# Optimization experiments

Hardware: AMD Instinct MI355X
Metric: run time of the kernel (lower is better)

## Reference

```python
import jax, jax.numpy as jnp
import numpy as np

T, B, H, I = 128, 128, 256, 256


def setup_inputs() -> dict:
    key = jax.random.key(0)
    ks = jax.random.split(key, 8)
    s = 1.0 / np.sqrt(H)
    embs = jax.random.normal(ks[0], (T, B, I), jnp.float32)
    # lens in [1, T] (a length of 0 is meaningless for this module)
    lens = jnp.maximum(jax.random.randint(ks[1], (B,), 0, T + 1), 1)
    Wih = jax.random.uniform(ks[2], (4 * H, I), jnp.float32, -s, s)
    Whh = jax.random.uniform(ks[3], (4 * H, H), jnp.float32, -s, s)
    bih = jax.random.uniform(ks[4], (4 * H,), jnp.float32, -s, s)
    bhh = jax.random.uniform(ks[5], (4 * H,), jnp.float32, -s, s)
    Wa = jax.random.uniform(ks[6], (H, 2 * H), jnp.float32, -s, s)
    ba = jnp.zeros((H,), jnp.float32)
    return {"embs": embs, "lens": lens, "Wih": Wih, "Whh": Whh,
            "bih": bih, "bhh": bhh, "Wa": Wa, "ba": ba}


def _forward(embs, Wih, Whh, bih, bhh, Wa, ba):
    Tn, Bn, _ = embs.shape
    Hn = Whh.shape[1]
    h0 = jnp.zeros((Bn, Hn), embs.dtype)
    c0 = jnp.zeros((Bn, Hn), embs.dtype)
    hids0 = jnp.zeros((Tn, Bn, Hn), embs.dtype)  # growing history of outputs
    pos = jnp.arange(Tn)

    def step(carry, emb):
        h, c, hids, t = carry
        # attention of current hidden over all previous outputs (dot-product scores)
        scores = jnp.einsum('bh,tbh->tb', h, hids)          # [T,B]
        valid = pos[:, None] < jnp.maximum(t, 1)             # at least one valid slot avoids NaN
        scores = jnp.where(valid, scores, -1e30)
        w = jax.nn.softmax(scores, axis=0)
        ctx = jnp.einsum('tb,tbh->bh', w, hids)              # [B,H]
        h_att = jnp.tanh(jnp.concatenate([h, ctx], axis=-1) @ Wa.T + ba)
        h_in = jnp.where(t > 0, h_att, h)                    # no attention before first output
        # one LSTM cell step (PyTorch gate order: i, f, g, o)
        gates = emb @ Wih.T + bih + h_in @ Whh.T + bhh       # [B,4H]
        i, f, g, o = jnp.split(gates, 4, axis=-1)
        c_new = jax.nn.sigmoid(f) * c + jax.nn.sigmoid(i) * jnp.tanh(g)
        h_new = jax.nn.sigmoid(o) * jnp.tanh(c_new)
        hids = jax.lax.dynamic_update_slice(hids, h_new[None], (t, 0, 0))
        return (h_new, c_new, hids, t + 1), (h_new, c_new)

    _, (hs, cs) = jax.lax.scan(step, (h0, c0, hids0, jnp.int32(0)), embs)
    return hs, cs  # each [T,B,H]


def reference(embs, lens, Wih, Whh, bih, bhh, Wa, ba):
    hs, cs = _forward(embs, Wih, Whh, bih, bhh, Wa, ba)
    bidx = jnp.arange(hs.shape[1])
    h_fin = hs[lens - 1, bidx][None]  # [1,B,H], state at t == len-1
    c_fin = cs[lens - 1, bidx][None]
    return hs, h_fin, c_fin
```

## Files before the change

### kernel.cpp

```cpp
#include <hip/hip_runtime.h>
#include <math.h>

#define T 128
#define B 128
#define H 256
#define I 256
#define G4 1024

typedef unsigned short u16;
typedef unsigned int u32;

__device__ __forceinline__ float2 bf2_to_f2(u32 u) {
    union { u32 i; float f; } a, b;
    a.i = u << 16;
    b.i = u & 0xffff0000u;
    return make_float2(a.f, b.f);
}

__device__ __forceinline__ u16 bf16_rne(float f) {
    union { float f; u32 u; } x; x.f = f;
    u32 r = x.u + 0x7fffu + ((x.u >> 16) & 1u);
    return (u16)(r >> 16);
}

__device__ __forceinline__ float sigmoid_fast(float x) {
    return 1.0f / (1.0f + __expf(-x));
}
__device__ __forceinline__ float tanh_fast(float x) {
    x = fminf(fmaxf(x, -15.f), 15.f);
    const float e = __expf(2.0f * x);
    return (e - 1.0f) / (e + 1.0f);
}

__global__ void pack_whB(const float* __restrict__ Whh, u16* __restrict__ WhB) {
    const int k = blockIdx.x;
    const int o = threadIdx.x;
    WhB[(size_t)k * G4 + o] = bf16_rne(Whh[(size_t)o * H + k]);
}
__global__ void pack_waB(const float* __restrict__ Wa, u16* __restrict__ WaB) {
    const int k = blockIdx.x;
    const int j = threadIdx.x;
    WaB[(size_t)k * H + j] = bf16_rne(Wa[(size_t)j * (2 * H) + k]);
}

__global__ __launch_bounds__(256) void gemm_g(const float* __restrict__ A,
                                              const float* __restrict__ W,
                                              const float* __restrict__ bih,
                                              const float* __restrict__ bhh,
                                              float* __restrict__ G) {
    __shared__ __align__(16) float As[64][68];
    __shared__ __align__(16) float Ws[64][68];
    const int m0 = blockIdx.x * 64;
    const int n0 = blockIdx.y * 64;
    const int tid = threadIdx.x;
    const int ty = tid >> 4, tx = tid & 15;
    const int rr = tid >> 4;
    const int kr = tid & 15;

    float acc[4][4] = {};
    for (int k0 = 0; k0 < I; k0 += 64) {
#pragma unroll
        for (int i = 0; i < 4; ++i) {
            const int r = rr + 16 * i;
            const float4 av = *(const float4*)&A[(size_t)(m0 + r) * I + k0 + kr * 4];
            const float4 wv = *(const float4*)&W[(size_t)(n0 + r) * I + k0 + kr * 4];
            As[kr * 4 + 0][r] = av.x; As[kr * 4 + 1][r] = av.y;
            As[kr * 4 + 2][r] = av.z; As[kr * 4 + 3][r] = av.w;
            Ws[kr * 4 + 0][r] = wv.x; Ws[kr * 4 + 1][r] = wv.y;
            Ws[kr * 4 + 2][r] = wv.z; Ws[kr * 4 + 3][r] = wv.w;
        }
        __syncthreads();
#pragma unroll 8
        for (int kk = 0; kk < 64; ++kk) {
            const float4 a4 = *(const float4*)&As[kk][ty * 4];
            const float4 w4 = *(const float4*)&Ws[kk][tx * 4];
            const float a[4] = {a4.x, a4.y, a4.z, a4.w};
            const float w[4] = {w4.x, w4.y, w4.z, w4.w};
#pragma unroll
            for (int i = 0; i < 4; ++i)
#pragma unroll
                for (int jj = 0; jj < 4; ++jj)
                    acc[i][jj] = fmaf(a[i], w[jj], acc[i][jj]);
        }
        __syncthreads();
    }
    const int n = n0 + tx * 4;
    const float4 bi = *(const float4*)&bih[n];
    const float4 bh = *(const float4*)&bhh[n];
    const float4 bb = make_float4(bi.x + bh.x, bi.y + bh.y, bi.z + bh.z, bi.w + bh.w);
#pragma unroll
    for (int i = 0; i < 4; ++i) {
        const int m = m0 + ty * 4 + i;
        float4 o = make_float4(acc[i][0] + bb.x, acc[i][1] + bb.y,
                               acc[i][2] + bb.z, acc[i][3] + bb.w);
        *(float4*)&G[(size_t)m * G4 + n] = o;
    }
}

__global__ __launch_bounds__(1024, 4) void alstm2(
    const int* __restrict__ lens,
    const float* __restrict__ G,
    const u16* __restrict__ WhB,
    const u16* __restrict__ WaB,
    const float* __restrict__ ba,
    float* __restrict__ out)
{
    __shared__ __align__(16) float hid_s[T][H];
    __shared__ __align__(16) float red_s[4096];
    __shared__ __align__(16) float gate_s[G4];
    __shared__ __align__(16) float h_s[H];
    __shared__ __align__(16) float hin_s[H];
    __shared__ __align__(16) float ctx_s[H];
    __shared__ __align__(16) float sc_s[T];

    const int b = blockIdx.x;
    const int tid = threadIdx.x;
    const int lane = tid & 63;
    const int wave = tid >> 6;
    const int len_b = lens[b];

    const int ko_h = tid >> 8;
    const int jo_h = tid & 255;
    const int ko_a = tid >> 6;
    const int jo_a = tid & 63;

    float c_reg = 0.f;
    const float ba_j = (tid < H) ? ba[tid] : 0.f;
    if (tid < H) h_s[tid] = 0.f;
    float* hs_out = out;
    float* hfin = out + (size_t)T * B * H;
    float* cfin = hfin + (size_t)B * H;
    __syncthreads();

    for (int t = 0; t < T; ++t) {
        if (t > 0) {
            const float4 h4 = *(const float4*)&h_s[lane * 4];
            for (int tp = wave; tp < t; tp += 16) {
                const float4 hv = *(const float4*)&hid_s[tp][lane * 4];
                float d = hv.x * h4.x + hv.y * h4.y + hv.z * h4.z + hv.w * h4.w;
#pragma unroll
                for (int off = 32; off; off >>= 1) d += __shfl_xor(d, off);
                if (lane == 0) sc_s[tp] = d;
            }
            __syncthreads();
            if (wave == 0) {
                const float v0 = (lane < t) ? sc_s[lane] : -3.0e38f;
                const float v1 = (lane + 64 < t) ? sc_s[lane + 64] : -3.0e38f;
                float m = fmaxf(v0, v1);
#pragma unroll
                for (int off = 32; off; off >>= 1) m = fmaxf(m, __shfl_xor(m, off));
                const float e0 = (lane < t) ? __expf(v0 - m) : 0.f;
                const float e1 = (lane + 64 < t) ? __expf(v1 - m) : 0.f;
                float s = e0 + e1;
#pragma unroll
                for (int off = 32; off; off >>= 1) s += __shfl_xor(s, off);
                const float inv = 1.f / s;
                if (lane < t) sc_s[lane] = e0 * inv;
                if (lane + 64 < t) sc_s[lane + 64] = e1 * inv;
            }
            __syncthreads();
            {
                float cacc = 0.f;
                for (int tp = ko_h; tp < t; tp += 4)
                    cacc = fmaf(sc_s[tp], hid_s[tp][jo_h], cacc);
                red_s[ko_h * H + jo_h] = cacc;
            }
            __syncthreads();
            if (tid < H)
                ctx_s[tid] = red_s[tid] + red_s[H + tid] + red_s[2 * H + tid] + red_s[3 * H + tid];
            __syncthreads();
            {
                float a0 = 0.f, a1 = 0.f, a2 = 0.f, a3 = 0.f;
                const int kb = ko_a * 32;
#pragma unroll 8
                for (int kk = 0; kk < 32; ++kk) {
                    const int k = kb + kk;
                    const float vin = (k < H) ? h_s[k] : ctx_s[k - H];
                    const uint2 w = *(const uint2*)&WaB[(size_t)k * H + jo_a * 4];
                    const float2 w01 = bf2_to_f2(w.x), w23 = bf2_to_f2(w.y);
                    a0 = fmaf(w01.x, vin, a0); a1 = fmaf(w01.y, vin, a1);
                    a2 = fmaf(w23.x, vin, a2); a3 = fmaf(w23.y, vin, a3);
                }
                *(float4*)&red_s[ko_a * H + jo_a * 4] = make_float4(a0, a1, a2, a3);
            }
            __syncthreads();
            if (tid < H) {
                float a = ba_j;
#pragma unroll
                for (int r = 0; r < 16; ++r) a += red_s[r * H + tid];
                hin_s[tid] = tanh_fast(a);
            }
        } else {
            if (tid < H) hin_s[tid] = 0.f;
        }
        __syncthreads();
        {
            float g0 = 0.f, g1 = 0.f, g2 = 0.f, g3 = 0.f;
            const int kb = ko_h * 64;
#pragma unroll 8
            for (int kk = 0; kk < 64; ++kk) {
                const int k = kb + kk;
                const float hk = hin_s[k];
                const uint2 w = *(const uint2*)&WhB[(size_t)k * G4 + jo_h * 4];
                const float2 w01 = bf2_to_f2(w.x), w23 = bf2_to_f2(w.y);
                g0 = fmaf(w01.x, hk, g0); g1 = fmaf(w01.y, hk, g1);
                g2 = fmaf(w23.x, hk, g2); g3 = fmaf(w23.y, hk, g3);
            }
            *(float4*)&red_s[ko_h * G4 + jo_h * 4] = make_float4(g0, g1, g2, g3);
        }
        __syncthreads();
        {
            const float* Grow = G + (size_t)(t * B + b) * G4;
            gate_s[tid] = Grow[tid] + red_s[tid] + red_s[G4 + tid]
                        + red_s[2 * G4 + tid] + red_s[3 * G4 + tid];
        }
        __syncthreads();
        if (tid < H) {
            const float ig = sigmoid_fast(gate_s[tid]);
            const float fg = sigmoid_fast(gate_s[H + tid]);
            const float gg = tanh_fast(gate_s[2 * H + tid]);
            const float og = sigmoid_fast(gate_s[3 * H + tid]);
            c_reg = fmaf(fg, c_reg, ig * gg);
            const float h_new = og * tanh_fast(c_reg);
            h_s[tid] = h_new;
            hid_s[t][tid] = h_new;
            hs_out[(size_t)(t * B + b) * H + tid] = h_new;
            if (t == len_b - 1) {
                hfin[b * H + tid] = h_new;
                cfin[b * H + tid] = c_reg;
            }
        }
        __syncthreads();
    }
}

extern "C" void kernel_launch(void* const* d_in, const int* in_sizes, int n_in,
                              void* d_out, int out_size, void* d_ws, size_t ws_size,
                              hipStream_t stream) {
    const float* embs = (const float*)d_in[0];
    const int*   lens = (const int*)d_in[1];
    const float* Wih  = (const float*)d_in[2];
    const float* Whh  = (const float*)d_in[3];
    const float* bih  = (const float*)d_in[4];
    const float* bhh  = (const float*)d_in[5];
    const float* Wa   = (const float*)d_in[6];
    const float* ba   = (const float*)d_in[7];
    float* out = (float*)d_out;

    float* G  = (float*)d_ws;
    u16* WhB  = (u16*)(G + (size_t)T * B * G4);
    u16* WaB  = WhB + (size_t)H * G4;

    pack_whB<<<H, G4, 0, stream>>>(Whh, WhB);
    pack_waB<<<2 * H, H, 0, stream>>>(Wa, WaB);
    dim3 ggrid(T * B / 64, G4 / 64);
    gemm_g<<<ggrid, 256, 0, stream>>>(embs, Wih, bih, bhh, G);
    alstm2<<<B, 1024, 0, stream>>>(lens, G, WhB, WaB, ba, out);
}
```

Measured before the change: 2.078 ms.

## Process two batch rows per block with bf16 history and shared weight loads

```diff
diff --git a/kernel.cpp b/kernel.cpp
--- a/kernel.cpp
+++ b/kernel.cpp
@@ -6,6 +6,7 @@
 #define H 256
 #define I 256
 #define G4 1024
+#define NB 2
 
 typedef unsigned short u16;
 typedef unsigned int u32;
@@ -16,13 +17,14 @@
     b.i = u & 0xffff0000u;
     return make_float2(a.f, b.f);
 }
-
+__device__ __forceinline__ float bf1_to_f(u16 u) {
+    union { u32 i; float f; } a; a.i = ((u32)u) << 16; return a.f;
+}
 __device__ __forceinline__ u16 bf16_rne(float f) {
     union { float f; u32 u; } x; x.f = f;
     u32 r = x.u + 0x7fffu + ((x.u >> 16) & 1u);
     return (u16)(r >> 16);
 }
-
 __device__ __forceinline__ float sigmoid_fast(float x) {
     return 1.0f / (1.0f + __expf(-x));
 }
@@ -97,7 +99,7 @@
     }
 }
 
-__global__ __launch_bounds__(1024, 4) void alstm2(
+__global__ __launch_bounds__(1024, 4) void alstm3(
     const int* __restrict__ lens,
     const float* __restrict__ G,
     const u16* __restrict__ WhB,
@@ -105,47 +107,56 @@
     const float* __restrict__ ba,
     float* __restrict__ out)
 {
-    __shared__ __align__(16) float hid_s[T][H];
+    __shared__ __align__(16) u16   hid_s[NB][T][H];
     __shared__ __align__(16) float red_s[4096];
-    __shared__ __align__(16) float gate_s[G4];
-    __shared__ __align__(16) float h_s[H];
-    __shared__ __align__(16) float hin_s[H];
-    __shared__ __align__(16) float ctx_s[H];
-    __shared__ __align__(16) float sc_s[T];
-
-    const int b = blockIdx.x;
+    __shared__ __align__(16) float gate_s[NB][G4];
+    __shared__ __align__(16) float h_s[NB][H];
+    __shared__ __align__(16) float hin_s[NB][H];
+    __shared__ __align__(16) float ctx_s[NB][H];
+    __shared__ __align__(16) float sc_s[NB][T];
+
+    const int b0 = blockIdx.x * NB;
     const int tid = threadIdx.x;
     const int lane = tid & 63;
     const int wave = tid >> 6;
-    const int len_b = lens[b];
-
-    const int ko_h = tid >> 8;
-    const int jo_h = tid & 255;
-    const int ko_a = tid >> 6;
-    const int jo_a = tid & 63;
-
+    const int sb = wave >> 3;
+    const int stp0 = wave & 7;
+    const int cb = tid >> 9;
+    const int ck = (tid >> 8) & 1;
+    const int cj = tid & 255;
+    const int ako = tid >> 7;
+    const int aj = (tid & 127) * 2;
+    const int hko = tid >> 9;
+    const int ho = (tid & 511) * 2;
+    const int eb = tid >> 8;
+    const int ej = tid & 255;
+
+    const int len0 = lens[b0], len1 = lens[b0 + 1];
     float c_reg = 0.f;
-    const float ba_j = (tid < H) ? ba[tid] : 0.f;
-    if (tid < H) h_s[tid] = 0.f;
-    float* hs_out = out;
+    if (tid < NB * H) h_s[eb][ej] = 0.f;
     float* hfin = out + (size_t)T * B * H;
     float* cfin = hfin + (size_t)B * H;
     __syncthreads();
 
     for (int t = 0; t < T; ++t) {
+        const float gA = G[((size_t)t * B + b0) * G4 + tid];
+        const float gB = G[((size_t)t * B + b0 + 1) * G4 + tid];
+
         if (t > 0) {
-            const float4 h4 = *(const float4*)&h_s[lane * 4];
-            for (int tp = wave; tp < t; tp += 16) {
-                const float4 hv = *(const float4*)&hid_s[tp][lane * 4];
-                float d = hv.x * h4.x + hv.y * h4.y + hv.z * h4.z + hv.w * h4.w;
+            const float4 h4 = *(const float4*)&h_s[sb][lane * 4];
+            for (int tp = stp0; tp < t; tp += 8) {
+                const uint2 hv = *(const uint2*)&hid_s[sb][tp][lane * 4];
+                const float2 ha = bf2_to_f2(hv.x);
+                const float2 hb = bf2_to_f2(hv.y);
+                float d = ha.x * h4.x + ha.y * h4.y + hb.x * h4.z + hb.y * h4.w;
 #pragma unroll
                 for (int off = 32; off; off >>= 1) d += __shfl_xor(d, off);
-                if (lane == 0) sc_s[tp] = d;
-            }
-            __syncthreads();
-            if (wave == 0) {
-                const float v0 = (lane < t) ? sc_s[lane] : -3.0e38f;
-                const float v1 = (lane + 64 < t) ? sc_s[lane + 64] : -3.0e38f;
+                if (lane == 0) sc_s[sb][tp] = d;
+            }
+            __syncthreads();
+            if (stp0 == 0) {
+                const float v0 = (lane < t) ? sc_s[sb][lane] : -3.0e38f;
+                const float v1 = (lane + 64 < t) ? sc_s[sb][lane + 64] : -3.0e38f;
                 float m = fmaxf(v0, v1);
 #pragma unroll
                 for (int off = 32; off; off >>= 1) m = fmaxf(m, __shfl_xor(m, off));
@@ -155,79 +166,90 @@
 #pragma unroll
                 for (int off = 32; off; off >>= 1) s += __shfl_xor(s, off);
                 const float inv = 1.f / s;
-                if (lane < t) sc_s[lane] = e0 * inv;
-                if (lane + 64 < t) sc_s[lane + 64] = e1 * inv;
+                if (lane < t) sc_s[sb][lane] = e0 * inv;
+                if (lane + 64 < t) sc_s[sb][lane + 64] = e1 * inv;
             }
             __syncthreads();
             {
                 float cacc = 0.f;
-                for (int tp = ko_h; tp < t; tp += 4)
-                    cacc = fmaf(sc_s[tp], hid_s[tp][jo_h], cacc);
-                red_s[ko_h * H + jo_h] = cacc;
-            }
-            __syncthreads();
-            if (tid < H)
-                ctx_s[tid] = red_s[tid] + red_s[H + tid] + red_s[2 * H + tid] + red_s[3 * H + tid];
+#pragma unroll 4
+                for (int tp = ck; tp < t; tp += 2)
+                    cacc = fmaf(sc_s[cb][tp], bf1_to_f(hid_s[cb][tp][cj]), cacc);
+                red_s[cb * 512 + ck * 256 + cj] = cacc;
+                gate_s[0][tid] = gA;
+                gate_s[1][tid] = gB;
+            }
+            __syncthreads();
+            if (tid < 512)
+                ctx_s[eb][ej] = red_s[eb * 512 + ej] + red_s[eb * 512 + 256 + ej];
             __syncthreads();
             {
-                float a0 = 0.f, a1 = 0.f, a2 = 0.f, a3 = 0.f;
-                const int kb = ko_a * 32;
+                const float* base0 = (ako < 4) ? &h_s[0][ako * 64] : &ctx_s[0][ako * 64 - 256];
+                const float* base1 = (ako < 4) ? &h_s[1][ako * 64] : &ctx_s[1][ako * 64 - 256];
+                const u16* wp = &WaB[(size_t)(ako * 64) * H + aj];
+                float a00 = 0.f, a01 = 0.f, a10 = 0.f, a11 = 0.f;
 #pragma unroll 8
-                for (int kk = 0; kk < 32; ++kk) {
-                    const int k = kb + kk;
-                    const float vin = (k < H) ? h_s[k] : ctx_s[k - H];
-                    const uint2 w = *(const uint2*)&WaB[(size_t)k * H + jo_a * 4];
-                    const float2 w01 = bf2_to_f2(w.x), w23 = bf2_to_f2(w.y);
-                    a0 = fmaf(w01.x, vin, a0); a1 = fmaf(w01.y, vin, a1);
-                    a2 = fmaf(w23.x, vin, a2); a3 = fmaf(w23.y, vin, a3);
+                for (int kk = 0; kk < 64; ++kk) {
+                    const u32 w = *(const u32*)(wp + (size_t)kk * H);
+                    const float2 wv = bf2_to_f2(w);
+                    const float v0 = base0[kk];
+                    const float v1 = base1[kk];
+                    a00 = fmaf(wv.x, v0, a00); a01 = fmaf(wv.y, v0, a01);
+                    a10 = fmaf(wv.x, v1, a10); a11 = fmaf(wv.y, v1, a11);
                 }
-                *(float4*)&red_s[ko_a * H + jo_a * 4] = make_float4(a0, a1, a2, a3);
-            }
-            __syncthreads();
-            if (tid < H) {
-                float a = ba_j;
-#pragma unroll
-                for (int r = 0; r < 16; ++r) a += red_s[r * H + tid];
-                hin_s[tid] = tanh_fast(a);
-            }
+                *(float2*)&red_s[ako * 512 + aj] = make_float2(a00, a01);
+                *(float2*)&red_s[ako * 512 + 256 + aj] = make_float2(a10, a11);
+            }
+            __syncthreads();
+            if (tid < 512) {
+                float a = ba[ej];
+#pragma unroll
+                for (int r = 0; r < 8; ++r) a += red_s[r * 512 + eb * 256 + ej];
+                hin_s[eb][ej] = tanh_fast(a);
+            }
+            __syncthreads();
         } else {
-            if (tid < H) hin_s[tid] = 0.f;
-        }
-        __syncthreads();
+            gate_s[0][tid] = gA;
+            gate_s[1][tid] = gB;
+            if (tid < 512) hin_s[eb][ej] = 0.f;
+            __syncthreads();
+        }
         {
-            float g0 = 0.f, g1 = 0.f, g2 = 0.f, g3 = 0.f;
-            const int kb = ko_h * 64;
+            const u16* wp = &WhB[(size_t)(hko * 128) * G4 + ho];
+            float a00 = 0.f, a01 = 0.f, a10 = 0.f, a11 = 0.f;
 #pragma unroll 8
-            for (int kk = 0; kk < 64; ++kk) {
-                const int k = kb + kk;
-                const float hk = hin_s[k];
-                const uint2 w = *(const uint2*)&WhB[(size_t)k * G4 + jo_h * 4];
-                const float2 w01 = bf2_to_f2(w.x), w23 = bf2_to_f2(w.y);
-                g0 = fmaf(w01.x, hk, g0); g1 = fmaf(w01.y, hk, g1);
-                g2 = fmaf(w23.x, hk, g2); g3 = fmaf(w23.y, hk, g3);
-            }
-            *(float4*)&red_s[ko_h * G4 + jo_h * 4] = make_float4(g0, g1, g2, g3);
-        }
-        __syncthreads();
-        {
-            const float* Grow = G + (size_t)(t * B + b) * G4;
-            gate_s[tid] = Grow[tid] + red_s[tid] + red_s[G4 + tid]
-                        + red_s[2 * G4 + tid] + red_s[3 * G4 + tid];
-        }
-        __syncthreads();
-        if (tid < H) {
-            const float ig = sigmoid_fast(gate_s[tid]);
-            const float fg = sigmoid_fast(gate_s[H + tid]);
-            const float gg = tanh_fast(gate_s[2 * H + tid]);
-            const float og = sigmoid_fast(gate_s[3 * H + tid]);
-            c_reg = fmaf(fg, c_reg, ig * gg);
+            for (int kk = 0; kk < 128; ++kk) {
+                const int k = hko * 128 + kk;
+                const u32 w = *(const u32*)(wp + (size_t)kk * G4);
+                const float2 wv = bf2_to_f2(w);
+                const float h0 = hin_s[0][k];
+                const float h1 = hin_s[1][k];
+                a00 = fmaf(wv.x, h0, a00); a01 = fmaf(wv.y, h0, a01);
+                a10 = fmaf(wv.x, h1, a10); a11 = fmaf(wv.y, h1, a11);
+            }
+            *(float2*)&red_s[hko * 2048 + ho] = make_float2(a00, a01);
+            *(float2*)&red_s[hko * 2048 + 1024 + ho] = make_float2(a10, a11);
+        }
+        __syncthreads();
+        if (tid < 512) {
+            const int bg = b0 + eb;
+            const float gi = gate_s[eb][ej] + red_s[eb * 1024 + ej] + red_s[2048 + eb * 1024 + ej];
+            const float gf = gate_s[eb][H + ej] + red_s[eb * 1024 + H + ej] + red_s[2048 + eb * 1024 + H + ej];
+            const float gg = gate_s[eb][2 * H + ej] + red_s[eb * 1024 + 2 * H + ej] + red_s[2048 + eb * 1024 + 2 * H + ej];
+            const float go = gate_s[eb][3 * H + ej] + red_s[eb * 1024 + 3 * H + ej] + red_s[2048 + eb * 1024 + 3 * H + ej];
+            const float ig = sigmoid_fast(gi);
+            const float fg = sigmoid_fast(gf);
+            const float gv = tanh_fast(gg);
+            const float og = sigmoid_fast(go);
+            c_reg = fmaf(fg, c_reg, ig * gv);
             const float h_new = og * tanh_fast(c_reg);
-            h_s[tid] = h_new;
-            hid_s[t][tid] = h_new;
-            hs_out[(size_t)(t * B + b) * H + tid] = h_new;
-            if (t == len_b - 1) {
-                hfin[b * H + tid] = h_new;
-                cfin[b * H + tid] = c_reg;
+            h_s[eb][ej] = h_new;
+            hid_s[eb][t][ej] = bf16_rne(h_new);
+            out[((size_t)t * B + bg) * H + ej] = h_new;
+            const int lb = eb ? len1 : len0;
+            if (t == lb - 1) {
+                hfin[(size_t)bg * H + ej] = h_new;
+                cfin[(size_t)bg * H + ej] = c_reg;
             }
         }
         __syncthreads();
@@ -255,5 +277,5 @@
     pack_waB<<<2 * H, H, 0, stream>>>(Wa, WaB);
     dim3 ggrid(T * B / 64, G4 / 64);
     gemm_g<<<ggrid, 256, 0, stream>>>(embs, Wih, bih, bhh, G);
-    alstm2<<<B, 1024, 0, stream>>>(lens, G, WhB, WaB, ba, out);
-}
+    alstm3<<<B / NB, 1024, 0, stream>>>(lens, G, WhB, WaB, ba, out);
+}
```

Measured after the change: 2.043 ms. Within noise of the previous version (-1.7%).
